# Performance work log

Hardware: AMD Instinct MI355X
Metric: run time of the kernel (lower is better)

The kernel has to match this reference:

```python
import jax, jax.numpy as jnp
import numpy as np

IMG_DIM = 256
AUD_DIM = 256
N_HEADS = 8


def _linear_params(key, fan_in, fan_out):
    k1, k2 = jax.random.split(key)
    lim = 1.0 / np.sqrt(fan_in)
    W = jax.random.uniform(k1, (fan_in, fan_out), minval=-lim, maxval=lim, dtype=jnp.float32)
    b = jax.random.uniform(k2, (fan_out,), minval=-lim, maxval=lim, dtype=jnp.float32)
    return W, b


def setup_inputs() -> dict:
    key = jax.random.key(0)
    ks = jax.random.split(key, 16)
    B, Nv, Na = 16, 1024, 512
    inp = {
        "image_feat": jax.random.normal(ks[0], (B, Nv, IMG_DIM), dtype=jnp.float32),
        "audio_feat": jax.random.normal(ks[1], (B, Na, AUD_DIM), dtype=jnp.float32),
    }
    inp["Wq_i"], inp["bq_i"] = _linear_params(ks[2], IMG_DIM, IMG_DIM)
    inp["Wk_i"], inp["bk_i"] = _linear_params(ks[3], IMG_DIM, IMG_DIM)
    inp["Wv_i"], inp["bv_i"] = _linear_params(ks[4], IMG_DIM, IMG_DIM)
    inp["Wo_i"], inp["bo_i"] = _linear_params(ks[5], AUD_DIM, IMG_DIM)  # out_proj_image
    inp["Wq_a"], inp["bq_a"] = _linear_params(ks[6], AUD_DIM, AUD_DIM)
    inp["Wk_a"], inp["bk_a"] = _linear_params(ks[7], AUD_DIM, AUD_DIM)
    inp["Wv_a"], inp["bv_a"] = _linear_params(ks[8], AUD_DIM, AUD_DIM)
    inp["Wo_a"], inp["bo_a"] = _linear_params(ks[9], IMG_DIM, AUD_DIM)  # out_proj_audio
    inp["Wc1_i"], inp["bc1_i"] = _linear_params(ks[10], IMG_DIM + 2, IMG_DIM)
    inp["Wc2_i"], inp["bc2_i"] = _linear_params(ks[11], IMG_DIM, N_HEADS)
    inp["Wc1_a"], inp["bc1_a"] = _linear_params(ks[12], AUD_DIM + 2, AUD_DIM)
    inp["Wc2_a"], inp["bc2_a"] = _linear_params(ks[13], AUD_DIM, N_HEADS)
    inp["Wg_i"], inp["bg_i"] = _linear_params(ks[14], IMG_DIM, IMG_DIM)
    inp["Wg_a"], inp["bg_a"] = _linear_params(ks[15], AUD_DIM, AUD_DIM)
    return inp


def _heads(x, W, b, H):
    # x: [B, N, C] -> [B, H, N, C//H]
    B, N, _ = x.shape
    y = x @ W + b
    return y.reshape(B, N, H, -1).transpose(0, 2, 1, 3)


def _fwd(image_feat, audio_feat,
         Wq_i, bq_i, Wk_i, bk_i, Wv_i, bv_i, Wo_i, bo_i,
         Wq_a, bq_a, Wk_a, bk_a, Wv_a, bv_a, Wo_a, bo_a,
         Wc1_i, bc1_i, Wc2_i, bc2_i, Wc1_a, bc1_a, Wc2_a, bc2_a,
         Wg_i, bg_i, Wg_a, bg_a):
    H = N_HEADS
    B, Nv, Ci = image_feat.shape
    _, Na, Ca = audio_feat.shape
    scale_img = (Ci // H) ** (-0.5)
    scale_aud = (Ca // H) ** (-0.5)

    tp_img = image_feat.mean(axis=1)  # [B, Ci]
    tp_aud = audio_feat.mean(axis=1)  # [B, Ca]
    spatial_cond = jnp.linalg.norm(image_feat, axis=-1).mean(axis=1, keepdims=True)  # [B,1]
    time_cond = jnp.linalg.norm(audio_feat, axis=-1).mean(axis=1, keepdims=True)     # [B,1]

    # --- audio queries attend over image keys/values ---
    Q_a = _heads(audio_feat, Wq_a, bq_a, H)   # [B,H,Na,d]
    K_i = _heads(image_feat, Wk_i, bk_i, H)   # [B,H,Nv,d]
    V_i = _heads(image_feat, Wv_i, bv_i, H)   # [B,H,Nv,d]
    cond_aud = jnp.concatenate([tp_aud, spatial_cond, time_cond], axis=-1)  # [B,Ca+2]
    bias_a = (jax.nn.relu(cond_aud @ Wc1_a + bc1_a) @ Wc2_a + bc2_a)        # [B,H]
    logits_a = jnp.einsum('bhqd,bhkd->bhqk', Q_a, K_i) * scale_aud + bias_a[:, :, None, None]
    attn_a = jax.nn.softmax(logits_a, axis=-1)
    fused_a = jnp.einsum('bhqk,bhkd->bhqd', attn_a, V_i)  # [B,H,Na,d]
    fused_a = fused_a.transpose(0, 2, 1, 3).reshape(B, Na, Ci)
    fused_a = fused_a @ Wo_a + bo_a                        # [B,Na,Ca]
    gate_a = jax.nn.sigmoid(tp_aud @ Wg_a + bg_a)[:, None, :]
    audio_out = gate_a * fused_a + (1.0 - gate_a) * audio_feat

    # --- image queries attend over UPDATED audio keys/values ---
    Q_i = _heads(image_feat, Wq_i, bq_i, H)   # [B,H,Nv,d]
    K_a = _heads(audio_out, Wk_a, bk_a, H)    # [B,H,Na,d]
    V_a = _heads(audio_out, Wv_a, bv_a, H)    # [B,H,Na,d]
    cond_img = jnp.concatenate([tp_img, spatial_cond, time_cond], axis=-1)  # [B,Ci+2]
    bias_i = (jax.nn.relu(cond_img @ Wc1_i + bc1_i) @ Wc2_i + bc2_i)        # [B,H]
    logits_i = jnp.einsum('bhqd,bhkd->bhqk', Q_i, K_a) * scale_img + bias_i[:, :, None, None]
    attn_i = jax.nn.softmax(logits_i, axis=-1)
    fused_i = jnp.einsum('bhqk,bhkd->bhqd', attn_i, V_a)  # [B,H,Nv,d]
    fused_i = fused_i.transpose(0, 2, 1, 3).reshape(B, Nv, Ca)
    fused_i = fused_i @ Wo_i + bo_i                        # [B,Nv,Ci]
    gate_i = jax.nn.sigmoid(tp_img @ Wg_i + bg_i)[:, None, :]
    image_out = gate_i * fused_i + (1.0 - gate_i) * image_feat

    return image_out, audio_out


def reference(image_feat, audio_feat,
              Wq_i, bq_i, Wk_i, bk_i, Wv_i, bv_i, Wo_i, bo_i,
              Wq_a, bq_a, Wk_a, bk_a, Wv_a, bv_a, Wo_a, bo_a,
              Wc1_i, bc1_i, Wc2_i, bc2_i, Wc1_a, bc1_a, Wc2_a, bc2_a,
              Wg_i, bg_i, Wg_a, bg_a):
    return _fwd(image_feat, audio_feat,
                Wq_i, bq_i, Wk_i, bk_i, Wv_i, bv_i, Wo_i, bo_i,
                Wq_a, bq_a, Wk_a, bk_a, Wv_a, bv_a, Wo_a, bo_a,
                Wc1_i, bc1_i, Wc2_i, bc2_i, Wc1_a, bc1_a, Wc2_a, bc2_a,
                Wg_i, bg_i, Wg_a, bg_a)
```

## Files before the change

### kernel.cpp

```cpp
#include <hip/hip_runtime.h>

#define C 256

typedef short s16x8 __attribute__((ext_vector_type(8)));
typedef float f32x4 __attribute__((ext_vector_type(4)));

#if __has_builtin(__builtin_amdgcn_exp2f)
#define EXP2F __builtin_amdgcn_exp2f
#else
#define EXP2F exp2f
#endif

__device__ __forceinline__ unsigned short f2b(float f) {
    unsigned u = __float_as_uint(f);
    unsigned r = (u + 0x7fffu + ((u >> 16) & 1u)) >> 16;
    return (unsigned short)r;
}

__device__ __forceinline__ unsigned pack2(float a, float b) {
    return __builtin_amdgcn_perm(__float_as_uint(b) + 0x8000u,
                                 __float_as_uint(a) + 0x8000u, 0x07060302u);
}

struct WPtrs { const float* src[8]; unsigned short* dst[8]; };

__device__ __forceinline__ void cast_mean_body(
    const float* __restrict__ x, unsigned short* __restrict__ y, float* __restrict__ part,
    int N, int nseg, int b, int seg, int tid) {
    __shared__ float red[4][C];
    int cg = tid & 63, rg = tid >> 6;
    int iters = nseg >> 2;
    const float* xp = x + ((size_t)b * N + (size_t)seg * nseg + rg) * C + cg * 4;
    unsigned short* yp = y + ((size_t)b * N + (size_t)seg * nseg + rg) * C + cg * 4;
    float s0 = 0.f, s1 = 0.f, s2 = 0.f, s3 = 0.f;
    for (int i = 0; i < iters; ++i) {
        float4 v = *(const float4*)(xp + (size_t)i * 4 * C);
        s0 += v.x; s1 += v.y; s2 += v.z; s3 += v.w;
        ushort4 o; o.x = f2b(v.x); o.y = f2b(v.y); o.z = f2b(v.z); o.w = f2b(v.w);
        *(ushort4*)(yp + (size_t)i * 4 * C) = o;
    }
    float4 s4 = {s0, s1, s2, s3};
    *(float4*)&red[rg][cg * 4] = s4;
    __syncthreads();
    float s = red[0][tid] + red[1][tid] + red[2][tid] + red[3][tid];
    part[(b * 8 + seg) * C + tid] = s;
}

__global__ void prep_kernel(const float* __restrict__ img, const float* __restrict__ aud,
                            unsigned short* __restrict__ R1, unsigned short* __restrict__ R4,
                            float* __restrict__ partI, float* __restrict__ partA, WPtrs wp) {
    int x = blockIdx.x, tid = threadIdx.x;
    if (x < 128) {
        cast_mean_body(img, R1, partI, 1024, 128, x >> 3, x & 7, tid);
    } else if (x < 256) {
        int id = x - 128;
        cast_mean_body(aud, R4, partA, 512, 64, id >> 3, id & 7, tid);
    } else {
        int id = x - 256;
        const float* W = wp.src[id >> 2];
        unsigned short* Wt = wp.dst[id >> 2];
        int n = (id & 3) * 64 + (tid & 63);
        int k0 = (tid >> 6) * 64;
#pragma unroll
        for (int kk = 0; kk < 64; kk += 4) {
            float a0 = W[(size_t)(k0 + kk + 0) * C + n];
            float a1 = W[(size_t)(k0 + kk + 1) * C + n];
            float a2 = W[(size_t)(k0 + kk + 2) * C + n];
            float a3 = W[(size_t)(k0 + kk + 3) * C + n];
            ushort4 o; o.x = f2b(a0); o.y = f2b(a1); o.z = f2b(a2); o.w = f2b(a3);
            *(ushort4*)(Wt + (size_t)n * C + k0 + kk) = o;
        }
    }
}

struct GDesc {
    const unsigned short* A;
    const unsigned short* Bt;
    const float* bias;
    unsigned short* Yh;
    int N;
    int start;
    int lnb;
    int bias_on_m;
    float oscale;
};
struct GArgs {
    GDesc d[4];
    int off1, off2, off3;
    int gemm_total;
    const float* partI; const float* partA;
    const float* WgI; const float* WgA;
    const float* bgI; const float* bgA;
    float* gI; float* gA;
    float invNv, invNa;
};

__global__ __launch_bounds__(256, 2) void gemm_multi(GArgs ga) {
    __shared__ unsigned short sA[128 * 40];
    __shared__ unsigned short sB[64 * 40];
    const int bid = blockIdx.x;
    const int tid = threadIdx.x;

    if (bid >= ga.gemm_total) {
        float* t = (float*)sA;
        int id = bid - ga.gemm_total;
        int b = id >> 1, which = id & 1;
        const float* part = which ? ga.partA : ga.partI;
        const float* Wg = which ? ga.WgA : ga.WgI;
        const float* bg = which ? ga.bgA : ga.bgI;
        float* g = which ? ga.gA : ga.gI;
        float invN = which ? ga.invNa : ga.invNv;
        float s = 0.f;
#pragma unroll
        for (int j = 0; j < 8; ++j) s += part[(b * 8 + j) * C + tid];
        t[tid] = s * invN;
        __syncthreads();
        float acc = bg[tid];
#pragma unroll 8
        for (int k = 0; k < C; ++k) acc += t[k] * Wg[k * C + tid];
        g[b * C + tid] = 1.f / (1.f + __expf(-acc));
        return;
    }

    const int j = (bid >= ga.off1) + (bid >= ga.off2) + (bid >= ga.off3);
    const GDesc d = ga.d[j];
    const int local = bid - d.start;
    const int bn = (local & ((1 << d.lnb) - 1)) * 64;
    const int bm = (local >> d.lnb) * 128;

    const int wave = tid >> 6, lane = tid & 63;
    const int quad = lane >> 4, l16 = lane & 15;
    const int ar0 = tid >> 2, ac0 = tid & 3;
    const int ar1 = (tid + 256) >> 2;
    const int br = tid >> 2, bc = tid & 3;

    f32x4 acc[2][4];
#pragma unroll
    for (int i = 0; i < 2; ++i)
#pragma unroll
        for (int k = 0; k < 4; ++k) acc[i][k] = (f32x4){0.f, 0.f, 0.f, 0.f};

    uint4 pa0 = *(const uint4*)(d.A + (size_t)(bm + ar0) * 256 + ac0 * 8);
    uint4 pa1 = *(const uint4*)(d.A + (size_t)(bm + ar1) * 256 + ac0 * 8);
    uint4 pb  = *(const uint4*)(d.Bt + (size_t)(bn + br) * 256 + bc * 8);

    for (int k0 = 0; k0 < 256; k0 += 32) {
        __syncthreads();
        *(uint4*)(sA + ar0 * 40 + ac0 * 8) = pa0;
        *(uint4*)(sA + ar1 * 40 + ac0 * 8) = pa1;
        *(uint4*)(sB + br * 40 + bc * 8) = pb;
        if (k0 < 224) {
            pa0 = *(const uint4*)(d.A + (size_t)(bm + ar0) * 256 + k0 + 32 + ac0 * 8);
            pa1 = *(const uint4*)(d.A + (size_t)(bm + ar1) * 256 + k0 + 32 + ac0 * 8);
            pb  = *(const uint4*)(d.Bt + (size_t)(bn + br) * 256 + k0 + 32 + bc * 8);
        }
        __syncthreads();
        s16x8 af[2], bf[4];
#pragma unroll
        for (int mt = 0; mt < 2; ++mt)
            af[mt] = *(const s16x8*)(sA + (wave * 32 + mt * 16 + l16) * 40 + quad * 8);
#pragma unroll
        for (int nt = 0; nt < 4; ++nt)
            bf[nt] = *(const s16x8*)(sB + (nt * 16 + l16) * 40 + quad * 8);
#pragma unroll
        for (int mt = 0; mt < 2; ++mt)
#pragma unroll
            for (int nt = 0; nt < 4; ++nt)
                acc[mt][nt] = __builtin_amdgcn_mfma_f32_16x16x32_bf16(af[mt], bf[nt], acc[mt][nt], 0, 0, 0);
    }

#pragma unroll
    for (int mt = 0; mt < 2; ++mt) {
#pragma unroll
        for (int nt = 0; nt < 4; ++nt) {
            int n = bn + nt * 16 + l16;
            float bias_n = d.bias_on_m ? 0.f : d.bias[n];
#pragma unroll
            for (int r = 0; r < 4; ++r) {
                int m = bm + wave * 32 + mt * 16 + quad * 4 + r;
                float y = acc[mt][nt][r] + (d.bias_on_m ? d.bias[m] : bias_n);
                d.Yh[(size_t)m * d.N + n] = f2b(y * d.oscale);
            }
        }
    }
}

template <bool STORE_BF16>
__global__ __launch_bounds__(256, 2) void gemm_out(
    const unsigned short* __restrict__ A, const unsigned short* __restrict__ Bt,
    const float* __restrict__ bias, float* __restrict__ Yf, unsigned short* __restrict__ Yh,
    int M, const float* __restrict__ gate, const float* __restrict__ resid, int rows_per_b) {
    __shared__ unsigned short sA[128 * 40];
    __shared__ unsigned short sB[64 * 40];
    const int tid = threadIdx.x;
    const int wave = tid >> 6, lane = tid & 63;
    const int quad = lane >> 4, l16 = lane & 15;
    const int bm = blockIdx.y * 128, bn = blockIdx.x * 64;
    const int ar0 = tid >> 2, ac0 = tid & 3;
    const int ar1 = (tid + 256) >> 2;
    const int br = tid >> 2, bc = tid & 3;

    f32x4 acc[2][4];
#pragma unroll
    for (int i = 0; i < 2; ++i)
#pragma unroll
        for (int k = 0; k < 4; ++k) acc[i][k] = (f32x4){0.f, 0.f, 0.f, 0.f};

    uint4 pa0 = *(const uint4*)(A + (size_t)(bm + ar0) * 256 + ac0 * 8);
    uint4 pa1 = *(const uint4*)(A + (size_t)(bm + ar1) * 256 + ac0 * 8);
    uint4 pb  = *(const uint4*)(Bt + (size_t)(bn + br) * 256 + bc * 8);

    for (int k0 = 0; k0 < 256; k0 += 32) {
        __syncthreads();
        *(uint4*)(sA + ar0 * 40 + ac0 * 8) = pa0;
        *(uint4*)(sA + ar1 * 40 + ac0 * 8) = pa1;
        *(uint4*)(sB + br * 40 + bc * 8) = pb;
        if (k0 < 224) {
            pa0 = *(const uint4*)(A + (size_t)(bm + ar0) * 256 + k0 + 32 + ac0 * 8);
            pa1 = *(const uint4*)(A + (size_t)(bm + ar1) * 256 + k0 + 32 + ac0 * 8);
            pb  = *(const uint4*)(Bt + (size_t)(bn + br) * 256 + k0 + 32 + bc * 8);
        }
        __syncthreads();
        s16x8 af[2], bf[4];
#pragma unroll
        for (int mt = 0; mt < 2; ++mt)
            af[mt] = *(const s16x8*)(sA + (wave * 32 + mt * 16 + l16) * 40 + quad * 8);
#pragma unroll
        for (int nt = 0; nt < 4; ++nt)
            bf[nt] = *(const s16x8*)(sB + (nt * 16 + l16) * 40 + quad * 8);
#pragma unroll
        for (int mt = 0; mt < 2; ++mt)
#pragma unroll
            for (int nt = 0; nt < 4; ++nt)
                acc[mt][nt] = __builtin_amdgcn_mfma_f32_16x16x32_bf16(af[mt], bf[nt], acc[mt][nt], 0, 0, 0);
    }

    const int b = bm / rows_per_b;
#pragma unroll
    for (int mt = 0; mt < 2; ++mt) {
#pragma unroll
        for (int nt = 0; nt < 4; ++nt) {
            int n = bn + nt * 16 + l16;
            float bias_n = bias[n];
            float g = gate[b * C + n];
#pragma unroll
            for (int r = 0; r < 4; ++r) {
                int m = bm + wave * 32 + mt * 16 + quad * 4 + r;
                float y = acc[mt][nt][r] + bias_n;
                float rv = resid[(size_t)m * C + n];
                y = g * y + (1.f - g) * rv;
                Yf[(size_t)m * C + n] = y;
                if (STORE_BF16) Yh[(size_t)m * C + n] = f2b(y);
            }
        }
    }
}

__global__ __launch_bounds__(256) void attn_mfma(
    const unsigned short* __restrict__ Q, const unsigned short* __restrict__ K,
    const unsigned short* __restrict__ Vt, unsigned short* __restrict__ O,
    int Nq, int Nk, int vtStride, int lnxb) {
    __shared__ unsigned short sK[64 * 40];
    __shared__ unsigned short sVt[32 * 72];
    __shared__ unsigned short sP[4][16 * 40];
    const int tid = threadIdx.x;
    const int wave = tid >> 6, lane = tid & 63;
    const int quad = lane >> 4, l16 = lane & 15;
    const int id = blockIdx.x;
    const int slot = id >> 3;
    const int bh = (id & 7) + 8 * (slot >> lnxb);
    const int xb = slot & ((1 << lnxb) - 1);
    const int b = bh >> 3, h = bh & 7;
    const int q0 = xb * 64 + wave * 16;

    s16x8 qf = *(const s16x8*)(Q + ((size_t)b * Nq + q0 + l16) * 256 + h * 32 + quad * 8);
    f32x4 oacc[2];
    oacc[0] = (f32x4){0.f, 0.f, 0.f, 0.f};
    oacc[1] = (f32x4){0.f, 0.f, 0.f, 0.f};
    float rs = 0.f;

    const int kr = tid >> 2, kc = tid & 3;
    const int vr = tid >> 3, vc = tid & 7;
    const unsigned short* Kb = K + (size_t)b * Nk * 256 + h * 32;
    const unsigned short* Vb = Vt + (size_t)(h * 32 + vr) * vtStride + (size_t)b * Nk;

    uint4 ka = *(const uint4*)(Kb + (size_t)kr * 256 + kc * 8);
    uint4 va = *(const uint4*)(Vb + vc * 8);
    const int n1 = (64 < Nk) ? 64 : 0;
    uint4 kb = *(const uint4*)(Kb + (size_t)(n1 + kr) * 256 + kc * 8);
    uint4 vb = *(const uint4*)(Vb + n1 + vc * 8);

    for (int k0 = 0; k0 < Nk; k0 += 64) {
        __syncthreads();
        *(uint4*)(sK + kr * 40 + kc * 8) = ka;
        *(uint4*)(sVt + vr * 72 + vc * 8) = va;
        ka = kb; va = vb;
        int np = k0 + 128; if (np >= Nk) np = Nk - 64;
        kb = *(const uint4*)(Kb + (size_t)(np + kr) * 256 + kc * 8);
        vb = *(const uint4*)(Vb + np + vc * 8);
        __syncthreads();

        unsigned short* p = &sP[wave][0];
#pragma unroll
        for (int kg = 0; kg < 2; ++kg) {
#pragma unroll
            for (int kt = 0; kt < 2; ++kt) {
                s16x8 kf = *(const s16x8*)(sK + (kg * 32 + kt * 16 + l16) * 40 + quad * 8);
                f32x4 z = (f32x4){0.f, 0.f, 0.f, 0.f};
                f32x4 st = __builtin_amdgcn_mfma_f32_16x16x32_bf16(kf, qf, z, 0, 0, 0);
                float p0 = EXP2F(st[0]), p1 = EXP2F(st[1]);
                float p2 = EXP2F(st[2]), p3 = EXP2F(st[3]);
                rs += (p0 + p1) + (p2 + p3);
                uint2 pk;
                pk.x = pack2(p0, p1);
                pk.y = pack2(p2, p3);
                *(uint2*)(p + l16 * 40 + kt * 16 + quad * 4) = pk;
            }
            s16x8 pf = *(const s16x8*)(p + l16 * 40 + quad * 8);
#pragma unroll
            for (int dh = 0; dh < 2; ++dh) {
                s16x8 vf = *(const s16x8*)(sVt + (dh * 16 + l16) * 72 + kg * 32 + quad * 8);
                oacc[dh] = __builtin_amdgcn_mfma_f32_16x16x32_bf16(pf, vf, oacc[dh], 0, 0, 0);
            }
        }
    }

    rs += __shfl_xor(rs, 16, 64);
    rs += __shfl_xor(rs, 32, 64);
    float inv = 1.f / rs;
#pragma unroll
    for (int rr = 0; rr < 4; ++rr) {
        float iq = __shfl(inv, quad * 4 + rr, 64);
#pragma unroll
        for (int dh = 0; dh < 2; ++dh)
            O[((size_t)b * Nq + q0 + quad * 4 + rr) * 256 + h * 32 + dh * 16 + l16] =
                f2b(oacc[dh][rr] * iq);
    }
}

extern "C" void kernel_launch(void* const* d_in, const int* in_sizes, int n_in,
                              void* d_out, int out_size, void* d_ws, size_t ws_size,
                              hipStream_t stream) {
    (void)in_sizes; (void)n_in; (void)out_size; (void)ws_size;
    const float* img  = (const float*)d_in[0];
    const float* aud  = (const float*)d_in[1];
    const float* Wq_i = (const float*)d_in[2];  const float* bq_i = (const float*)d_in[3];
    const float* Wk_i = (const float*)d_in[4];  const float* bk_i = (const float*)d_in[5];
    const float* Wv_i = (const float*)d_in[6];  const float* bv_i = (const float*)d_in[7];
    const float* Wo_i = (const float*)d_in[8];  const float* bo_i = (const float*)d_in[9];
    const float* Wq_a = (const float*)d_in[10]; const float* bq_a = (const float*)d_in[11];
    const float* Wk_a = (const float*)d_in[12]; const float* bk_a = (const float*)d_in[13];
    const float* Wv_a = (const float*)d_in[14]; const float* bv_a = (const float*)d_in[15];
    const float* Wo_a = (const float*)d_in[16]; const float* bo_a = (const float*)d_in[17];
    const float* Wg_i = (const float*)d_in[26]; const float* bg_i = (const float*)d_in[27];
    const float* Wg_a = (const float*)d_in[28]; const float* bg_a = (const float*)d_in[29];

    const int B = 16, Nv = 1024, Na = 512;
    const int Mi = B * Nv, Ma = B * Na;
    const size_t MiC = (size_t)Mi * C;
    const size_t MaC = (size_t)Ma * C;

    float* out_img = (float*)d_out;
    float* out_aud = out_img + MiC;

    unsigned short* wsu = (unsigned short*)d_ws;
    unsigned short* R1 = wsu;
    unsigned short* R2 = R1 + MiC;
    unsigned short* R3 = R2 + MiC;
    unsigned short* R8 = R3 + MiC;
    unsigned short* R4 = R8 + MiC;
    unsigned short* R5 = R4 + MaC;
    unsigned short* R6 = R5 + MaC;
    unsigned short* R7 = R6 + MaC;
    unsigned short* wt = R7 + MaC;
    float* fws   = (float*)(wt + 8 * 65536);
    float* partI = fws;
    float* partA = partI + B * 8 * C;
    float* gI    = partA + B * 8 * C;
    float* gA    = gI + B * C;

    unsigned short* wtQa = wt + 0 * 65536;
    unsigned short* wtKi = wt + 1 * 65536;
    unsigned short* wtVi = wt + 2 * 65536;
    unsigned short* wtOa = wt + 3 * 65536;
    unsigned short* wtKa = wt + 4 * 65536;
    unsigned short* wtVa = wt + 5 * 65536;
    unsigned short* wtQi = wt + 6 * 65536;
    unsigned short* wtOi = wt + 7 * 65536;

    const float qs = 0.17677669529663687f * 1.4426950408889634f;
    dim3 blk(256);

    WPtrs wp;
    wp.src[0] = Wq_a; wp.dst[0] = wtQa;
    wp.src[1] = Wk_i; wp.dst[1] = wtKi;
    wp.src[2] = Wv_i; wp.dst[2] = wtVi;
    wp.src[3] = Wo_a; wp.dst[3] = wtOa;
    wp.src[4] = Wk_a; wp.dst[4] = wtKa;
    wp.src[5] = Wv_a; wp.dst[5] = wtVa;
    wp.src[6] = Wq_i; wp.dst[6] = wtQi;
    wp.src[7] = Wo_i; wp.dst[7] = wtOi;
    prep_kernel<<<288, blk, 0, stream>>>(img, aud, R1, R4, partI, partA, wp);

    GArgs g1 = {};
    g1.d[0] = {R4,   wtQa, bq_a, R5, 256,   0,    2, 0, qs };
    g1.d[1] = {R1,   wtKi, bk_i, R2, 256,   256,  2, 0, 1.f};
    g1.d[2] = {wtVi, R1,   bv_i, R3, 16384, 768,  8, 1, 1.f};
    g1.d[3] = {R1,   wtQi, bq_i, R8, 256,   1280, 2, 0, qs };
    g1.off1 = 256; g1.off2 = 768; g1.off3 = 1280; g1.gemm_total = 1792;
    g1.partI = partI; g1.partA = partA;
    g1.WgI = Wg_i; g1.WgA = Wg_a; g1.bgI = bg_i; g1.bgA = bg_a;
    g1.gI = gI; g1.gA = gA; g1.invNv = 1.f / Nv; g1.invNa = 1.f / Na;
    gemm_multi<<<1792 + 32, blk, 0, stream>>>(g1);

    attn_mfma<<<128 * (Na / 64), blk, 0, stream>>>(R5, R2, R3, R6, Na, Nv, Mi, 3);

    gemm_out<true><<<dim3(4, Ma / 128), blk, 0, stream>>>(R6, wtOa, bo_a, out_aud, R7, Ma, gA, aud, Na);

    GArgs g2 = {};
    g2.d[0] = {R7,   wtKa, bk_a, R5, 256,  0,   2, 0, 1.f};
    g2.d[1] = {wtVa, R7,   bv_a, R6, 8192, 256, 7, 1, 1.f};
    g2.off1 = 256; g2.off2 = 512; g2.off3 = 512; g2.gemm_total = 512;
    gemm_multi<<<512, blk, 0, stream>>>(g2);

    attn_mfma<<<128 * (Nv / 64), blk, 0, stream>>>(R8, R5, R6, R2, Nv, Na, Ma, 4);

    gemm_out<false><<<dim3(4, Mi / 128), blk, 0, stream>>>(R2, wtOi, bo_i, out_img, nullptr, Mi, gI, img, Nv);
}
```

Baseline: 241.7 us.

## Process two query tiles per wave in attention to reuse K/V loads

Templates the attention kernel on Q2 and has each wave handle two 16-row query tiles, so each block covers 128 queries. Every K/V tile staged in shared memory and every K/V fragment read from it now feeds twice as many MFMAs, halving the grid size and the global K/V traffic. The cost is more registers and shared memory per block and half as many blocks, which could reduce occupancy or leave some CUs idle.

```diff
diff --git a/kernel.cpp b/kernel.cpp
--- a/kernel.cpp
+++ b/kernel.cpp
@@ -256,13 +256,14 @@
     }
 }
 
+template <int Q2>
 __global__ __launch_bounds__(256) void attn_mfma(
     const unsigned short* __restrict__ Q, const unsigned short* __restrict__ K,
     const unsigned short* __restrict__ Vt, unsigned short* __restrict__ O,
     int Nq, int Nk, int vtStride, int lnxb) {
     __shared__ unsigned short sK[64 * 40];
     __shared__ unsigned short sVt[32 * 72];
-    __shared__ unsigned short sP[4][16 * 40];
+    __shared__ unsigned short sP[4][Q2][16 * 40];
     const int tid = threadIdx.x;
     const int wave = tid >> 6, lane = tid & 63;
     const int quad = lane >> 4, l16 = lane & 15;
@@ -271,13 +272,18 @@
     const int bh = (id & 7) + 8 * (slot >> lnxb);
     const int xb = slot & ((1 << lnxb) - 1);
     const int b = bh >> 3, h = bh & 7;
-    const int q0 = xb * 64 + wave * 16;
-
-    s16x8 qf = *(const s16x8*)(Q + ((size_t)b * Nq + q0 + l16) * 256 + h * 32 + quad * 8);
-    f32x4 oacc[2];
-    oacc[0] = (f32x4){0.f, 0.f, 0.f, 0.f};
-    oacc[1] = (f32x4){0.f, 0.f, 0.f, 0.f};
-    float rs = 0.f;
+    const int q0 = xb * (64 * Q2) + wave * (16 * Q2);
+
+    s16x8 qf[Q2];
+    f32x4 oacc[Q2][2];
+    float rs[Q2];
+#pragma unroll
+    for (int q = 0; q < Q2; ++q) {
+        qf[q] = *(const s16x8*)(Q + ((size_t)b * Nq + q0 + q * 16 + l16) * 256 + h * 32 + quad * 8);
+        oacc[q][0] = (f32x4){0.f, 0.f, 0.f, 0.f};
+        oacc[q][1] = (f32x4){0.f, 0.f, 0.f, 0.f};
+        rs[q] = 0.f;
+    }
 
     const int kr = tid >> 2, kc = tid & 3;
     const int vr = tid >> 3, vc = tid & 7;
@@ -300,41 +306,49 @@
         vb = *(const uint4*)(Vb + np + vc * 8);
         __syncthreads();
 
-        unsigned short* p = &sP[wave][0];
-#pragma unroll
-        for (int kg = 0; kg < 2; ++kg) {
-#pragma unroll
-            for (int kt = 0; kt < 2; ++kt) {
-                s16x8 kf = *(const s16x8*)(sK + (kg * 32 + kt * 16 + l16) * 40 + quad * 8);
+#pragma unroll
+        for (int kt = 0; kt < 4; ++kt) {
+            s16x8 kf = *(const s16x8*)(sK + (kt * 16 + l16) * 40 + quad * 8);
+#pragma unroll
+            for (int q = 0; q < Q2; ++q) {
                 f32x4 z = (f32x4){0.f, 0.f, 0.f, 0.f};
-                f32x4 st = __builtin_amdgcn_mfma_f32_16x16x32_bf16(kf, qf, z, 0, 0, 0);
+                f32x4 st = __builtin_amdgcn_mfma_f32_16x16x32_bf16(kf, qf[q], z, 0, 0, 0);
                 float p0 = EXP2F(st[0]), p1 = EXP2F(st[1]);
                 float p2 = EXP2F(st[2]), p3 = EXP2F(st[3]);
-                rs += (p0 + p1) + (p2 + p3);
+                rs[q] += (p0 + p1) + (p2 + p3);
                 uint2 pk;
                 pk.x = pack2(p0, p1);
                 pk.y = pack2(p2, p3);
-                *(uint2*)(p + l16 * 40 + kt * 16 + quad * 4) = pk;
+                *(uint2*)(&sP[wave][q][0] + l16 * 40 + kt * 16 + quad * 4) = pk;
             }
-            s16x8 pf = *(const s16x8*)(p + l16 * 40 + quad * 8);
-#pragma unroll
-            for (int dh = 0; dh < 2; ++dh) {
-                s16x8 vf = *(const s16x8*)(sVt + (dh * 16 + l16) * 72 + kg * 32 + quad * 8);
-                oacc[dh] = __builtin_amdgcn_mfma_f32_16x16x32_bf16(pf, vf, oacc[dh], 0, 0, 0);
+        }
+#pragma unroll
+        for (int kg = 0; kg < 2; ++kg) {
+            s16x8 vf0 = *(const s16x8*)(sVt + l16 * 72 + kg * 32 + quad * 8);
+            s16x8 vf1 = *(const s16x8*)(sVt + (16 + l16) * 72 + kg * 32 + quad * 8);
+#pragma unroll
+            for (int q = 0; q < Q2; ++q) {
+                s16x8 pf = *(const s16x8*)(&sP[wave][q][0] + l16 * 40 + kg * 32 + quad * 8);
+                oacc[q][0] = __builtin_amdgcn_mfma_f32_16x16x32_bf16(pf, vf0, oacc[q][0], 0, 0, 0);
+                oacc[q][1] = __builtin_amdgcn_mfma_f32_16x16x32_bf16(pf, vf1, oacc[q][1], 0, 0, 0);
             }
         }
     }
 
-    rs += __shfl_xor(rs, 16, 64);
-    rs += __shfl_xor(rs, 32, 64);
-    float inv = 1.f / rs;
-#pragma unroll
-    for (int rr = 0; rr < 4; ++rr) {
-        float iq = __shfl(inv, quad * 4 + rr, 64);
-#pragma unroll
-        for (int dh = 0; dh < 2; ++dh)
-            O[((size_t)b * Nq + q0 + quad * 4 + rr) * 256 + h * 32 + dh * 16 + l16] =
-                f2b(oacc[dh][rr] * iq);
+#pragma unroll
+    for (int q = 0; q < Q2; ++q) {
+        float r = rs[q];
+        r += __shfl_xor(r, 16, 64);
+        r += __shfl_xor(r, 32, 64);
+        float inv = 1.f / r;
+#pragma unroll
+        for (int rr = 0; rr < 4; ++rr) {
+            float iq = __shfl(inv, quad * 4 + rr, 64);
+#pragma unroll
+            for (int dh = 0; dh < 2; ++dh)
+                O[((size_t)b * Nq + q0 + q * 16 + quad * 4 + rr) * 256 + h * 32 + dh * 16 + l16] =
+                    f2b(oacc[q][dh][rr] * iq);
+        }
     }
 }
 
@@ -413,7 +427,7 @@
     g1.gI = gI; g1.gA = gA; g1.invNv = 1.f / Nv; g1.invNa = 1.f / Na;
     gemm_multi<<<1792 + 32, blk, 0, stream>>>(g1);
 
-    attn_mfma<<<128 * (Na / 64), blk, 0, stream>>>(R5, R2, R3, R6, Na, Nv, Mi, 3);
+    attn_mfma<2><<<128 * (Na / 128), blk, 0, stream>>>(R5, R2, R3, R6, Na, Nv, Mi, 2);
 
     gemm_out<true><<<dim3(4, Ma / 128), blk, 0, stream>>>(R6, wtOa, bo_a, out_aud, R7, Ma, gA, aud, Na);
 
@@ -423,7 +437,7 @@
     g2.off1 = 256; g2.off2 = 512; g2.off3 = 512; g2.gemm_total = 512;
     gemm_multi<<<512, blk, 0, stream>>>(g2);
 
-    attn_mfma<<<128 * (Nv / 64), blk, 0, stream>>>(R8, R5, R6, R2, Nv, Na, Ma, 4);
+    attn_mfma<2><<<128 * (Nv / 128), blk, 0, stream>>>(R8, R5, R6, R2, Nv, Na, Ma, 3);
 
     gemm_out<false><<<dim3(4, Mi / 128), blk, 0, stream>>>(R2, wtOi, bo_i, out_img, nullptr, Mi, gI, img, Nv);
 }
```

After: 243.9 us. About the same (+0.9%).
